# Kernel optimization log

Measured on AMD Instinct MI355X. Metric: run time of the kernel, lower is better.

The kernel has to match this reference:

```python
import jax, jax.numpy as jnp
import numpy as np

B, NMASK, DIM, HEADS = 8, 1024, 768, 12
HEAD_DIM = DIM // HEADS
SCALE = HEAD_DIM ** -0.5
NEG = -1e9  # finite stand-in for -inf to keep fully-masked rows NaN-free


def setup_inputs() -> dict:
    key = jax.random.key(0)
    ks = jax.random.split(key, 7)
    x = jax.random.normal(ks[0], (B, NMASK + 1, DIM), dtype=jnp.float32)
    # valid-prefix padding mask (realistic variable-length batch), lengths >= 1
    lengths = jax.random.randint(ks[1], (B,), 1, NMASK + 1)
    mask = jnp.arange(NMASK)[None, :] < lengths[:, None]  # (B, NMASK) bool
    w_qkv = jax.random.normal(ks[2], (DIM, 3 * DIM), dtype=jnp.float32) * (DIM ** -0.5)
    b_qkv = jax.random.normal(ks[3], (3 * DIM,), dtype=jnp.float32) * 0.02
    w_proj = jax.random.normal(ks[4], (DIM, DIM), dtype=jnp.float32) * (DIM ** -0.5)
    b_proj = jax.random.normal(ks[5], (DIM,), dtype=jnp.float32) * 0.02
    return {"x": x, "mask": mask, "w_qkv": w_qkv, "b_qkv": b_qkv,
            "w_proj": w_proj, "b_proj": b_proj}


def reference(x, mask, w_qkv, b_qkv, w_proj, b_proj):
    b, n, _ = x.shape
    qkv = x @ w_qkv + b_qkv                        # (b, n, 3*dim)
    qkv = qkv.reshape(b, n, 3, HEADS, HEAD_DIM)    # 'b n (qkv h d)'
    qkv = jnp.transpose(qkv, (2, 0, 3, 1, 4))      # (3, b, h, n, d)
    q, k, v = qkv[0], qkv[1], qkv[2]
    logits = jnp.einsum('bhid,bhjd->bhij', q, k) * SCALE
    m = jnp.pad(mask, ((0, 0), (1, 0)), constant_values=True)   # prepend CLS=True
    am = m[:, None, :] & m[:, :, None]             # (b, n, n)
    logits = jnp.where(am[:, None, :, :], logits, NEG)
    attn = jax.nn.softmax(logits, axis=-1)
    out = jnp.einsum('bhij,bhjd->bhid', attn, v)   # (b, h, n, d)
    out = jnp.transpose(out, (0, 2, 1, 3)).reshape(b, n, DIM)
    return out @ w_proj + b_proj                   # dropout is identity (eval/p=0)
```

## Files before the change

kernel.cpp:

```cpp
#include <hip/hip_runtime.h>
#include <stdint.h>

#define BATCH   8
#define NMASK_  1024
#define SEQ     1025
#define NPAD    1056
#define DIM     768
#define HEADS   12
#define HD      64
#define BHN     (BATCH*HEADS)
#define MROWS   (BATCH*SEQ)
#define K3      (3*DIM)

typedef unsigned short u16;
typedef __attribute__((ext_vector_type(8))) short s8v;
typedef __attribute__((ext_vector_type(4))) float f4v;
typedef __attribute__((ext_vector_type(4))) unsigned short u16x4;

__device__ __forceinline__ u16 rne_bf16(float f) {
  unsigned u = __float_as_uint(f);
  u += 0x7fffu + ((u >> 16) & 1u);
  return (u16)(u >> 16);
}
__device__ __forceinline__ float bf2f(u16 u) {
  return __uint_as_float(((unsigned)u) << 16);
}

__device__ __forceinline__ void gld16(const u16* g, u16* l) {
  __builtin_amdgcn_global_load_lds(
      (const __attribute__((address_space(1))) void*)g,
      (__attribute__((address_space(3))) void*)l, 16, 0, 0);
}

__global__ __launch_bounds__(256) void k_len(const int* __restrict__ mask,
                                             int* __restrict__ lens) {
  int b = blockIdx.x, t = threadIdx.x;
  int s = 0;
  for (int j = t; j < NMASK_; j += 256) s += (mask[b * NMASK_ + j] != 0) ? 1 : 0;
  __shared__ int red[256];
  red[t] = s; __syncthreads();
  for (int st = 128; st > 0; st >>= 1) { if (t < st) red[t] += red[t + st]; __syncthreads(); }
  if (t == 0) lens[b] = red[0] + 1;
}

__global__ __launch_bounds__(256) void k_cvt_x(const float* __restrict__ x,
                                               u16* __restrict__ xb, int n4) {
  int i = blockIdx.x * 256 + threadIdx.x;
  if (i >= n4) return;
  float4 v = ((const float4*)x)[i];
  u16x4 o;
  o[0] = rne_bf16(v.x); o[1] = rne_bf16(v.y); o[2] = rne_bf16(v.z); o[3] = rne_bf16(v.w);
  *(u16x4*)&xb[i * 4] = o;
}

__global__ __launch_bounds__(256) void k_wT(const float* __restrict__ w,
                                            u16* __restrict__ wT, int R, int C) {
  __shared__ float tile[32][33];
  int c0 = blockIdx.x * 32, r0 = blockIdx.y * 32;
  int tx = threadIdx.x & 31, ty = threadIdx.x >> 5;
  #pragma unroll
  for (int i = 0; i < 32; i += 8) tile[ty + i][tx] = w[(size_t)(r0 + ty + i) * C + c0 + tx];
  __syncthreads();
  #pragma unroll
  for (int i = 0; i < 32; i += 8)
    wT[(size_t)(c0 + ty + i) * R + r0 + tx] = rne_bf16(tile[tx][ty + i]);
}

__global__ __launch_bounds__(256) void k_zpad(u16* __restrict__ VT) {
  int idx = blockIdx.x * 256 + threadIdx.x;
  const int PADW = NPAD - SEQ;
  if (idx >= BHN * HD * PADW) return;
  int c = idx % PADW, rd = idx / PADW;
  VT[(size_t)rd * NPAD + SEQ + c] = 0;
}

__device__ __forceinline__ void gemm_ml128(const u16* __restrict__ A,
                                           const u16* __restrict__ Bt,
                                           int M, int m0, int n0,
                                           f4v acc[4][4], u16* smem) {
  u16* lA = smem;
  u16* lB = smem + 4096;
  const int t = threadIdx.x;
  const int w = t >> 6, l = t & 63, lg = l >> 4, lr = l & 15;
  const int wr = w >> 1, wc = w & 1;

  int rA0 = m0 + (t >> 2);       if (rA0 >= M) rA0 = M - 1;
  int rA1 = m0 + (t >> 2) + 64;  if (rA1 >= M) rA1 = M - 1;
  const u16* sA0 = A  + (size_t)rA0 * DIM + (t & 3) * 8;
  const u16* sA1 = A  + (size_t)rA1 * DIM + (t & 3) * 8;
  const u16* sB0 = Bt + (size_t)(n0 + (t >> 2)) * DIM + (t & 3) * 8;
  const u16* sB1 = Bt + (size_t)(n0 + (t >> 2) + 64) * DIM + (t & 3) * 8;
  u16* dA0 = &lA[w * 512];
  u16* dA1 = &lA[2048 + w * 512];
  u16* dB0 = &lB[w * 512];
  u16* dB1 = &lB[2048 + w * 512];

  #pragma unroll
  for (int fm = 0; fm < 4; fm++)
    #pragma unroll
    for (int fn = 0; fn < 4; fn++) { f4v z = {0.f, 0.f, 0.f, 0.f}; acc[fm][fn] = z; }

  for (int k0 = 0; k0 < DIM; k0 += 32) {
    __syncthreads();
    gld16(sA0, dA0); gld16(sA1, dA1);
    gld16(sB0, dB0); gld16(sB1, dB1);
    sA0 += 32; sA1 += 32; sB0 += 32; sB1 += 32;
    __syncthreads();
    s8v a[4], bb[4];
    #pragma unroll
    for (int fm = 0; fm < 4; fm++) a[fm] = *(const s8v*)&lA[(wr * 64 + fm * 16 + lr) * 32 + lg * 8];
    #pragma unroll
    for (int fn = 0; fn < 4; fn++) bb[fn] = *(const s8v*)&lB[(wc * 64 + fn * 16 + lr) * 32 + lg * 8];
    #pragma unroll
    for (int fm = 0; fm < 4; fm++)
      #pragma unroll
      for (int fn = 0; fn < 4; fn++)
        acc[fm][fn] = __builtin_amdgcn_mfma_f32_16x16x32_bf16(a[fm], bb[fn], acc[fm][fn], 0, 0, 0);
  }
}

__global__ __launch_bounds__(256) void k_gemm_qkv(const u16* __restrict__ xb,
                                                  const u16* __restrict__ wqkvT,
                                                  const float* __restrict__ bqkv,
                                                  const int* __restrict__ lens,
                                                  u16* __restrict__ Q,
                                                  u16* __restrict__ Kb,
                                                  u16* __restrict__ VT) {
  __shared__ alignas(16) u16 smem[16384];
  int m0 = blockIdx.x * 128, n0 = blockIdx.y * 128;
  const int which = n0 / DIM;
  if (which < 2) {
    int b0 = m0 / SEQ, off = m0 - b0 * SEQ;
    bool spans = (m0 + 127) >= (b0 + 1) * SEQ;
    if (!spans && off >= lens[b0]) return;
  }
  f4v acc[4][4];
  gemm_ml128(xb, wqkvT, MROWS, m0, n0, acc, smem);
  const int t = threadIdx.x;
  const int w = t >> 6, l = t & 63, lg = l >> 4, lr = l & 15;
  const int wr = w >> 1, wc = w & 1;
  const int hbase = (n0 - which * DIM) >> 6;
  const float qs = (which == 0) ? 0.125f : 1.0f;

  __syncthreads();
  #pragma unroll
  for (int fn = 0; fn < 4; fn++) {
    int col = wc * 64 + fn * 16 + lr;
    float bias = bqkv[n0 + col];
    #pragma unroll
    for (int fm = 0; fm < 4; fm++)
      #pragma unroll
      for (int r = 0; r < 4; r++) {
        int row = wr * 64 + fm * 16 + lg * 4 + r;
        smem[row * 128 + col] = rne_bf16((acc[fm][fn][r] + bias) * qs);
      }
  }
  __syncthreads();

  if (which < 2) {
    u16* dst = (which == 0) ? Q : Kb;
    #pragma unroll
    for (int p = 0; p < 8; p++) {
      int c = p * 256 + t;
      int row = c >> 4, col = (c & 15) * 8;
      int gm = m0 + row;
      if (gm >= MROWS) continue;
      int b = gm / SEQ, n = gm - b * SEQ;
      int head = hbase + (col >> 6), d = col & 63;
      *(s8v*)&dst[((size_t)(b * HEADS + head) * NPAD + n) * HD + d] =
          *(const s8v*)&smem[row * 128 + col];
    }
  } else {
    #pragma unroll
    for (int p = 0; p < 8; p++) {
      int c = p * 256 + t;
      int d = c & 127, nb = c >> 7;
      int gm0 = m0 + nb * 8;
      if (gm0 >= MROWS) continue;
      int head = hbase + (d >> 6), dl = d & 63;
      int b0 = gm0 / SEQ;
      if (gm0 + 7 < MROWS && (gm0 + 7) < (b0 + 1) * SEQ) {
        s8v v;
        #pragma unroll
        for (int e = 0; e < 8; e++) v[e] = (short)smem[(nb * 8 + e) * 128 + d];
        int n = gm0 - b0 * SEQ;
        *(s8v*)&VT[((size_t)(b0 * HEADS + head) * HD + dl) * NPAD + n] = v;
      } else {
        for (int e = 0; e < 8; e++) {
          int gm = gm0 + e;
          if (gm >= MROWS) break;
          int b = gm / SEQ, n = gm - b * SEQ;
          VT[((size_t)(b * HEADS + head) * HD + dl) * NPAD + n] = smem[(nb * 8 + e) * 128 + d];
        }
      }
    }
  }
}

__global__ __launch_bounds__(256) void k_vmean(const u16* __restrict__ VT,
                                               float* __restrict__ vmean) {
  int bh = blockIdx.x, t = threadIdx.x;
  int d = t >> 2, part = t & 3;
  const u16* row = VT + (size_t)(bh * HD + d) * NPAD;
  float s = 0.f;
  for (int jc = part * 264; jc < part * 264 + 264; jc += 8) {
    if (jc + 8 <= SEQ) {
      s8v v = *(const s8v*)&row[jc];
      #pragma unroll
      for (int e = 0; e < 8; e++) s += bf2f((u16)v[e]);
    } else {
      for (int e = 0; e < 8; e++) if (jc + e < SEQ) s += bf2f(row[jc + e]);
    }
  }
  __shared__ float red[256];
  red[t] = s; __syncthreads();
  if (part == 0)
    vmean[bh * HD + d] = (red[t] + red[t + 1] + red[t + 2] + red[t + 3]) * (1.0f / (float)SEQ);
}

__global__ __launch_bounds__(256) void k_vproj(const float* __restrict__ vmean,
                                               const u16* __restrict__ wprojT,
                                               const float* __restrict__ bproj,
                                               float* __restrict__ vproj) {
  int gid = blockIdx.x * 4 + (threadIdx.x >> 6);
  if (gid >= BATCH * DIM) return;
  int b = gid / DIM, n = gid - b * DIM;
  int l = threadIdx.x & 63;
  const u16* wr = wprojT + (size_t)n * DIM;
  const float* vm = vmean + b * DIM;
  float s = 0.f;
  #pragma unroll
  for (int i = 0; i < DIM / 64; ++i)
    s += vm[l + i * 64] * bf2f(wr[l + i * 64]);
  #pragma unroll
  for (int off = 32; off >= 1; off >>= 1) s += __shfl_xor(s, off);
  if (l == 0) vproj[gid] = s + bproj[n];
}

__global__ __launch_bounds__(256) void k_attn(const u16* __restrict__ Q,
                                              const u16* __restrict__ Kb,
                                              const u16* __restrict__ VT,
                                              const int* __restrict__ lens,
                                              u16* __restrict__ aout) {
  int bh = blockIdx.y; int b = bh / HEADS, h = bh - b * HEADS;
  int Lp1 = lens[b];
  int q0 = blockIdx.x * 64;
  if (q0 >= Lp1) return;
  __shared__ alignas(16) u16 Kt[64 * 64];
  __shared__ alignas(16) u16 Vt[64 * 64];
  __shared__ alignas(16) u16 Pt[4][16 * 72];
  const int t = threadIdx.x, w = t >> 6, l = t & 63, lg = l >> 4, lr = l & 15;
  const u16* Qbh = Q  + (size_t)bh * NPAD * HD;
  const u16* Kbh = Kb + (size_t)bh * NPAD * HD;
  const u16* Vbh = VT + (size_t)bh * HD * NPAD;

  int qi = q0 + w * 16 + lr;
  s8v qf[2];
  qf[0] = *(const s8v*)&Qbh[(size_t)qi * HD +      lg * 8];
  qf[1] = *(const s8v*)&Qbh[(size_t)qi * HD + 32 + lg * 8];

  f4v o[4];
  #pragma unroll
  for (int fd = 0; fd < 4; fd++) { f4v z = {0.f, 0.f, 0.f, 0.f}; o[fd] = z; }
  float mrow[4], ssum[4];
  #pragma unroll
  for (int r = 0; r < 4; r++) { mrow[r] = -1e30f; ssum[r] = 0.f; }

  const int js = t >> 2, cs = t & 3;
  const u16* kSrc = Kbh + (size_t)js * HD   + cs * 8;
  const u16* vSrc = Vbh + (size_t)js * NPAD + cs * 8;
  const int kDst0 = js * 64 + ((cs       ^ (js & 7)) * 8);
  const int kDst1 = js * 64 + (((cs + 4) ^ (js & 7)) * 8);
  s8v kr0, kr1, vr0, vr1;
  kr0 = *(const s8v*)(kSrc);        kr1 = *(const s8v*)(kSrc + 32);
  vr0 = *(const s8v*)(vSrc);        vr1 = *(const s8v*)(vSrc + 32);

  for (int j0 = 0; j0 < Lp1; j0 += 64) {
    __syncthreads();
    *(s8v*)&Kt[kDst0] = kr0;  *(s8v*)&Kt[kDst1] = kr1;
    *(s8v*)&Vt[kDst0] = vr0;  *(s8v*)&Vt[kDst1] = vr1;
    if (j0 + 64 < Lp1) {
      kr0 = *(const s8v*)(kSrc + (size_t)(j0 + 64) * HD);
      kr1 = *(const s8v*)(kSrc + (size_t)(j0 + 64) * HD + 32);
      vr0 = *(const s8v*)(vSrc + (j0 + 64));
      vr1 = *(const s8v*)(vSrc + (j0 + 64) + 32);
    }
    __syncthreads();

    f4v sf[4];
    #pragma unroll
    for (int jf = 0; jf < 4; jf++) { f4v z = {0.f,0.f,0.f,0.f}; sf[jf] = z; }
    __builtin_amdgcn_s_setprio(1);
    #pragma unroll
    for (int jf = 0; jf < 4; jf++) {
      int j = jf * 16 + lr;
      #pragma unroll
      for (int kf = 0; kf < 2; kf++) {
        s8v kfr = *(const s8v*)&Kt[j * 64 + (((kf * 4 + lg) ^ (j & 7)) * 8)];
        sf[jf] = __builtin_amdgcn_mfma_f32_16x16x32_bf16(qf[kf], kfr, sf[jf], 0, 0, 0);
      }
    }
    __builtin_amdgcn_s_setprio(0);

    bool ok[4];
    #pragma unroll
    for (int jf = 0; jf < 4; jf++) ok[jf] = (j0 + jf * 16 + lr) < Lp1;

    float sv[4][4], pmax[4];
    #pragma unroll
    for (int r = 0; r < 4; r++) {
      float s0 = ok[0] ? sf[0][r] : -1e30f;
      float s1 = ok[1] ? sf[1][r] : -1e30f;
      float s2 = ok[2] ? sf[2][r] : -1e30f;
      float s3 = ok[3] ? sf[3][r] : -1e30f;
      sv[r][0] = s0; sv[r][1] = s1; sv[r][2] = s2; sv[r][3] = s3;
      float tm = fmaxf(fmaxf(s0, s1), fmaxf(s2, s3));
      tm = fmaxf(tm, __shfl_xor(tm, 1)); tm = fmaxf(tm, __shfl_xor(tm, 2));
      tm = fmaxf(tm, __shfl_xor(tm, 4)); tm = fmaxf(tm, __shfl_xor(tm, 8));
      pmax[r] = tm;
    }
    bool ng = (pmax[0] <= mrow[0] + 8.f) && (pmax[1] <= mrow[1] + 8.f) &&
              (pmax[2] <= mrow[2] + 8.f) && (pmax[3] <= mrow[3] + 8.f);
    if (!__all(ng)) {
      #pragma unroll
      for (int r = 0; r < 4; r++) {
        float nm = fmaxf(mrow[r], pmax[r]);
        float fs = __expf(mrow[r] - nm);
        mrow[r] = nm;
        ssum[r] *= fs;
        o[0][r] *= fs; o[1][r] *= fs; o[2][r] *= fs; o[3][r] *= fs;
      }
    }
    u16* P = &Pt[w][0];
    #pragma unroll
    for (int r = 0; r < 4; r++) {
      float e0 = __expf(sv[r][0] - mrow[r]);
      float e1 = __expf(sv[r][1] - mrow[r]);
      float e2 = __expf(sv[r][2] - mrow[r]);
      float e3 = __expf(sv[r][3] - mrow[r]);
      int prow = (lg * 4 + r) * 72;
      P[prow +      lr] = rne_bf16(e0);
      P[prow + 16 + lr] = rne_bf16(e1);
      P[prow + 32 + lr] = rne_bf16(e2);
      P[prow + 48 + lr] = rne_bf16(e3);
      float rs = (e0 + e1) + (e2 + e3);
      rs += __shfl_xor(rs, 1); rs += __shfl_xor(rs, 2);
      rs += __shfl_xor(rs, 4); rs += __shfl_xor(rs, 8);
      ssum[r] += rs;
    }
    asm volatile("s_waitcnt lgkmcnt(0)" ::: "memory");
    s8v pa[2];
    pa[0] = *(const s8v*)&P[lr * 72 +      lg * 8];
    pa[1] = *(const s8v*)&P[lr * 72 + 32 + lg * 8];
    __builtin_amdgcn_s_setprio(1);
    #pragma unroll
    for (int fd = 0; fd < 4; fd++) {
      int dv = fd * 16 + lr;
      #pragma unroll
      for (int kf = 0; kf < 2; kf++) {
        s8v vb = *(const s8v*)&Vt[dv * 64 + (((kf * 4 + lg) ^ (dv & 7)) * 8)];
        o[fd] = __builtin_amdgcn_mfma_f32_16x16x32_bf16(pa[kf], vb, o[fd], 0, 0, 0);
      }
    }
    __builtin_amdgcn_s_setprio(0);
  }

  float inv[4];
  #pragma unroll
  for (int r = 0; r < 4; r++) inv[r] = 1.0f / ssum[r];
  #pragma unroll
  for (int fd = 0; fd < 4; fd++)
    #pragma unroll
    for (int r = 0; r < 4; r++) {
      int i = q0 + w * 16 + lg * 4 + r;
      if (i < Lp1)
        aout[(size_t)(b * SEQ + i) * DIM + h * HD + fd * 16 + lr] = rne_bf16(o[fd][r] * inv[r]);
    }
}

__global__ __launch_bounds__(256) void k_bcast(const int* __restrict__ lens,
                                               const float* __restrict__ vproj,
                                               float* __restrict__ out) {
  int idx = blockIdx.x * 256 + threadIdx.x;
  if (idx >= MROWS * DIM / 4) return;
  int e4 = idx * 4;
  int b = e4 / (SEQ * DIM);
  int rem = e4 - b * (SEQ * DIM);
  int i = rem / DIM;
  if (i >= lens[b]) {
    int c = rem - i * DIM;
    const float* vp = &vproj[b * DIM + c];
    float4 v = { vp[0], vp[1], vp[2], vp[3] };
    ((float4*)out)[idx] = v;
  }
}

__global__ __launch_bounds__(256) void k_gemm_proj(const u16* __restrict__ aout,
                                                   const u16* __restrict__ wprojT,
                                                   const float* __restrict__ bproj,
                                                   const int* __restrict__ lens,
                                                   float* __restrict__ out) {
  __shared__ alignas(16) u16 smem[16384];
  int m0 = blockIdx.x * 128, n0 = blockIdx.y * 128;
  {
    int b0 = m0 / SEQ, off = m0 - b0 * SEQ;
    bool spans = (m0 + 127) >= (b0 + 1) * SEQ;
    if (!spans && off >= lens[b0]) return;
  }
  f4v acc[4][4];
  gemm_ml128(aout, wprojT, MROWS, m0, n0, acc, smem);
  const int t = threadIdx.x;
  const int w = t >> 6, l = t & 63, lg = l >> 4, lr = l & 15;
  const int wr = w >> 1, wc = w & 1;
  #pragma unroll
  for (int fn = 0; fn < 4; fn++) {
    int gc = n0 + wc * 64 + fn * 16 + lr;
    float bias = bproj[gc];
    #pragma unroll
    for (int fm = 0; fm < 4; fm++)
      #pragma unroll
      for (int r = 0; r < 4; r++) {
        int gm = m0 + wr * 64 + fm * 16 + lg * 4 + r;
        if (gm < MROWS) out[(size_t)gm * DIM + gc] = acc[fm][fn][r] + bias;
      }
  }
}

extern "C" void kernel_launch(void* const* d_in, const int* in_sizes, int n_in,
                              void* d_out, int out_size, void* d_ws, size_t ws_size,
                              hipStream_t stream) {
  const float* x      = (const float*)d_in[0];
  const int*   mask   = (const int*)  d_in[1];
  const float* w_qkv  = (const float*)d_in[2];
  const float* b_qkv  = (const float*)d_in[3];
  const float* w_proj = (const float*)d_in[4];
  const float* b_proj = (const float*)d_in[5];
  float* out = (float*)d_out;

  u16* xb     = (u16*)d_ws;
  u16* wqkvT  = xb    + (size_t)MROWS * DIM;
  u16* wprojT = wqkvT + (size_t)K3 * DIM;
  u16* Q      = wprojT + (size_t)DIM * DIM;
  u16* Kb     = Q     + (size_t)BHN * NPAD * HD;
  u16* VT     = Kb    + (size_t)BHN * NPAD * HD;
  float* vmean = (float*)(VT + (size_t)BHN * NPAD * HD);
  int* lens    = (int*)(vmean + BHN * HD);
  float* vproj = (float*)(lens + 256);
  u16* aout   = xb;

  k_len  <<<dim3(BATCH), dim3(256), 0, stream>>>(mask, lens);
  k_cvt_x<<<dim3((MROWS * DIM / 4 + 255) / 256), dim3(256), 0, stream>>>(x, xb, MROWS * DIM / 4);
  k_wT   <<<dim3(K3 / 32, DIM / 32), dim3(256), 0, stream>>>(w_qkv, wqkvT, DIM, K3);
  k_wT   <<<dim3(DIM / 32, DIM / 32), dim3(256), 0, stream>>>(w_proj, wprojT, DIM, DIM);
  k_zpad <<<dim3((BHN * HD * (NPAD - SEQ) + 255) / 256), dim3(256), 0, stream>>>(VT);
  k_gemm_qkv<<<dim3((MROWS + 127) / 128, K3 / 128), dim3(256), 0, stream>>>(xb, wqkvT, b_qkv, lens, Q, Kb, VT);
  k_vmean<<<dim3(BHN), dim3(256), 0, stream>>>(VT, vmean);
  k_vproj<<<dim3((BATCH * DIM + 3) / 4), dim3(256), 0, stream>>>(vmean, wprojT, b_proj, vproj);
  k_attn <<<dim3((SEQ + 63) / 64, BHN), dim3(256), 0, stream>>>(Q, Kb, VT, lens, aout);
  k_gemm_proj<<<dim3((MROWS + 127) / 128, DIM / 128), dim3(256), 0, stream>>>(aout, wprojT, b_proj, lens, out);
  k_bcast<<<dim3((MROWS * DIM / 4 + 255) / 256), dim3(256), 0, stream>>>(lens, vproj, out);
}
```

Baseline: 185.2 us.

## Process 128 query rows per attention block, reusing each K/V tile twice

Each wave in the attention kernel now handles two 16-row query sub-tiles instead of one, so a block covers 128 queries. Every K/V tile loaded into shared memory, and every V fragment read from it, serves twice as many MFMAs, which halves global K/V traffic and syncs per query. The grid is also reordered so bh is the fast dimension, spreading the variable-length batches across CUs. The cost is more registers per thread and fewer blocks, about 9 per head, which may lower occupancy and worsen load balance.

```diff
diff --git a/kernel.cpp b/kernel.cpp
--- a/kernel.cpp
+++ b/kernel.cpp
@@ -242,29 +242,36 @@
                                               const u16* __restrict__ VT,
                                               const int* __restrict__ lens,
                                               u16* __restrict__ aout) {
-  int bh = blockIdx.y; int b = bh / HEADS, h = bh - b * HEADS;
+  int bh = blockIdx.x; int b = bh / HEADS, h = bh - b * HEADS;
   int Lp1 = lens[b];
-  int q0 = blockIdx.x * 64;
+  int q0 = blockIdx.y * 128;
   if (q0 >= Lp1) return;
   __shared__ alignas(16) u16 Kt[64 * 64];
   __shared__ alignas(16) u16 Vt[64 * 64];
-  __shared__ alignas(16) u16 Pt[4][16 * 72];
+  __shared__ alignas(16) u16 Pt[4][32 * 72];
   const int t = threadIdx.x, w = t >> 6, l = t & 63, lg = l >> 4, lr = l & 15;
   const u16* Qbh = Q  + (size_t)bh * NPAD * HD;
   const u16* Kbh = Kb + (size_t)bh * NPAD * HD;
   const u16* Vbh = VT + (size_t)bh * HD * NPAD;
 
-  int qi = q0 + w * 16 + lr;
-  s8v qf[2];
-  qf[0] = *(const s8v*)&Qbh[(size_t)qi * HD +      lg * 8];
-  qf[1] = *(const s8v*)&Qbh[(size_t)qi * HD + 32 + lg * 8];
-
-  f4v o[4];
-  #pragma unroll
-  for (int fd = 0; fd < 4; fd++) { f4v z = {0.f, 0.f, 0.f, 0.f}; o[fd] = z; }
-  float mrow[4], ssum[4];
-  #pragma unroll
-  for (int r = 0; r < 4; r++) { mrow[r] = -1e30f; ssum[r] = 0.f; }
+  s8v qf[2][2];
+  #pragma unroll
+  for (int qa = 0; qa < 2; qa++) {
+    int qi = q0 + w * 32 + qa * 16 + lr;
+    qf[qa][0] = *(const s8v*)&Qbh[(size_t)qi * HD +      lg * 8];
+    qf[qa][1] = *(const s8v*)&Qbh[(size_t)qi * HD + 32 + lg * 8];
+  }
+
+  f4v o[2][4];
+  float mrow[2][4], ssum[2][4];
+  #pragma unroll
+  for (int qa = 0; qa < 2; qa++)
+    #pragma unroll
+    for (int fd = 0; fd < 4; fd++) { f4v z = {0.f, 0.f, 0.f, 0.f}; o[qa][fd] = z; }
+  #pragma unroll
+  for (int qa = 0; qa < 2; qa++)
+    #pragma unroll
+    for (int r = 0; r < 4; r++) { mrow[qa][r] = -1e30f; ssum[qa][r] = 0.f; }
 
   const int js = t >> 2, cs = t & 3;
   const u16* kSrc = Kbh + (size_t)js * HD   + cs * 8;
@@ -287,95 +294,107 @@
     }
     __syncthreads();
 
-    f4v sf[4];
-    #pragma unroll
-    for (int jf = 0; jf < 4; jf++) { f4v z = {0.f,0.f,0.f,0.f}; sf[jf] = z; }
-    __builtin_amdgcn_s_setprio(1);
-    #pragma unroll
-    for (int jf = 0; jf < 4; jf++) {
-      int j = jf * 16 + lr;
-      #pragma unroll
-      for (int kf = 0; kf < 2; kf++) {
-        s8v kfr = *(const s8v*)&Kt[j * 64 + (((kf * 4 + lg) ^ (j & 7)) * 8)];
-        sf[jf] = __builtin_amdgcn_mfma_f32_16x16x32_bf16(qf[kf], kfr, sf[jf], 0, 0, 0);
-      }
-    }
-    __builtin_amdgcn_s_setprio(0);
-
     bool ok[4];
     #pragma unroll
     for (int jf = 0; jf < 4; jf++) ok[jf] = (j0 + jf * 16 + lr) < Lp1;
-
-    float sv[4][4], pmax[4];
-    #pragma unroll
-    for (int r = 0; r < 4; r++) {
-      float s0 = ok[0] ? sf[0][r] : -1e30f;
-      float s1 = ok[1] ? sf[1][r] : -1e30f;
-      float s2 = ok[2] ? sf[2][r] : -1e30f;
-      float s3 = ok[3] ? sf[3][r] : -1e30f;
-      sv[r][0] = s0; sv[r][1] = s1; sv[r][2] = s2; sv[r][3] = s3;
-      float tm = fmaxf(fmaxf(s0, s1), fmaxf(s2, s3));
-      tm = fmaxf(tm, __shfl_xor(tm, 1)); tm = fmaxf(tm, __shfl_xor(tm, 2));
-      tm = fmaxf(tm, __shfl_xor(tm, 4)); tm = fmaxf(tm, __shfl_xor(tm, 8));
-      pmax[r] = tm;
-    }
-    bool ng = (pmax[0] <= mrow[0] + 8.f) && (pmax[1] <= mrow[1] + 8.f) &&
-              (pmax[2] <= mrow[2] + 8.f) && (pmax[3] <= mrow[3] + 8.f);
-    if (!__all(ng)) {
+    u16* P = &Pt[w][0];
+
+    #pragma unroll
+    for (int qa = 0; qa < 2; qa++) {
+      f4v sf[4];
+      #pragma unroll
+      for (int jf = 0; jf < 4; jf++) { f4v z = {0.f,0.f,0.f,0.f}; sf[jf] = z; }
+      __builtin_amdgcn_s_setprio(1);
+      #pragma unroll
+      for (int jf = 0; jf < 4; jf++) {
+        int j = jf * 16 + lr;
+        #pragma unroll
+        for (int kf = 0; kf < 2; kf++) {
+          s8v kfr = *(const s8v*)&Kt[j * 64 + (((kf * 4 + lg) ^ (j & 7)) * 8)];
+          sf[jf] = __builtin_amdgcn_mfma_f32_16x16x32_bf16(qf[qa][kf], kfr, sf[jf], 0, 0, 0);
+        }
+      }
+      __builtin_amdgcn_s_setprio(0);
+
+      float sv[4][4], pmax[4];
       #pragma unroll
       for (int r = 0; r < 4; r++) {
-        float nm = fmaxf(mrow[r], pmax[r]);
-        float fs = __expf(mrow[r] - nm);
-        mrow[r] = nm;
-        ssum[r] *= fs;
-        o[0][r] *= fs; o[1][r] *= fs; o[2][r] *= fs; o[3][r] *= fs;
-      }
-    }
-    u16* P = &Pt[w][0];
-    #pragma unroll
-    for (int r = 0; r < 4; r++) {
-      float e0 = __expf(sv[r][0] - mrow[r]);
-      float e1 = __expf(sv[r][1] - mrow[r]);
-      float e2 = __expf(sv[r][2] - mrow[r]);
-      float e3 = __expf(sv[r][3] - mrow[r]);
-      int prow = (lg * 4 + r) * 72;
-      P[prow +      lr] = rne_bf16(e0);
-      P[prow + 16 + lr] = rne_bf16(e1);
-      P[prow + 32 + lr] = rne_bf16(e2);
-      P[prow + 48 + lr] = rne_bf16(e3);
-      float rs = (e0 + e1) + (e2 + e3);
-      rs += __shfl_xor(rs, 1); rs += __shfl_xor(rs, 2);
-      rs += __shfl_xor(rs, 4); rs += __shfl_xor(rs, 8);
-      ssum[r] += rs;
-    }
+        float s0 = ok[0] ? sf[0][r] : -1e30f;
+        float s1 = ok[1] ? sf[1][r] : -1e30f;
+        float s2 = ok[2] ? sf[2][r] : -1e30f;
+        float s3 = ok[3] ? sf[3][r] : -1e30f;
+        sv[r][0] = s0; sv[r][1] = s1; sv[r][2] = s2; sv[r][3] = s3;
+        float tm = fmaxf(fmaxf(s0, s1), fmaxf(s2, s3));
+        tm = fmaxf(tm, __shfl_xor(tm, 1)); tm = fmaxf(tm, __shfl_xor(tm, 2));
+        tm = fmaxf(tm, __shfl_xor(tm, 4)); tm = fmaxf(tm, __shfl_xor(tm, 8));
+        pmax[r] = tm;
+      }
+      bool ng = (pmax[0] <= mrow[qa][0] + 8.f) && (pmax[1] <= mrow[qa][1] + 8.f) &&
+                (pmax[2] <= mrow[qa][2] + 8.f) && (pmax[3] <= mrow[qa][3] + 8.f);
+      if (!__all(ng)) {
+        #pragma unroll
+        for (int r = 0; r < 4; r++) {
+          float nm = fmaxf(mrow[qa][r], pmax[r]);
+          float fs = __expf(mrow[qa][r] - nm);
+          mrow[qa][r] = nm;
+          ssum[qa][r] *= fs;
+          o[qa][0][r] *= fs; o[qa][1][r] *= fs; o[qa][2][r] *= fs; o[qa][3][r] *= fs;
+        }
+      }
+      #pragma unroll
+      for (int r = 0; r < 4; r++) {
+        float e0 = __expf(sv[r][0] - mrow[qa][r]);
+        float e1 = __expf(sv[r][1] - mrow[qa][r]);
+        float e2 = __expf(sv[r][2] - mrow[qa][r]);
+        float e3 = __expf(sv[r][3] - mrow[qa][r]);
+        int prow = (qa * 16 + lg * 4 + r) * 72;
+        P[prow +      lr] = rne_bf16(e0);
+        P[prow + 16 + lr] = rne_bf16(e1);
+        P[prow + 32 + lr] = rne_bf16(e2);
+        P[prow + 48 + lr] = rne_bf16(e3);
+        float rs = (e0 + e1) + (e2 + e3);
+        rs += __shfl_xor(rs, 1); rs += __shfl_xor(rs, 2);
+        rs += __shfl_xor(rs, 4); rs += __shfl_xor(rs, 8);
+        ssum[qa][r] += rs;
+      }
+    }
+
     asm volatile("s_waitcnt lgkmcnt(0)" ::: "memory");
-    s8v pa[2];
-    pa[0] = *(const s8v*)&P[lr * 72 +      lg * 8];
-    pa[1] = *(const s8v*)&P[lr * 72 + 32 + lg * 8];
+    s8v pa[2][2];
+    #pragma unroll
+    for (int qa = 0; qa < 2; qa++) {
+      pa[qa][0] = *(const s8v*)&P[(qa * 16 + lr) * 72 +      lg * 8];
+      pa[qa][1] = *(const s8v*)&P[(qa * 16 + lr) * 72 + 32 + lg * 8];
+    }
     __builtin_amdgcn_s_setprio(1);
     #pragma unroll
     for (int fd = 0; fd < 4; fd++) {
       int dv = fd * 16 + lr;
-      #pragma unroll
-      for (int kf = 0; kf < 2; kf++) {
-        s8v vb = *(const s8v*)&Vt[dv * 64 + (((kf * 4 + lg) ^ (dv & 7)) * 8)];
-        o[fd] = __builtin_amdgcn_mfma_f32_16x16x32_bf16(pa[kf], vb, o[fd], 0, 0, 0);
+      s8v vb0 = *(const s8v*)&Vt[dv * 64 + (((0 * 4 + lg) ^ (dv & 7)) * 8)];
+      s8v vb1 = *(const s8v*)&Vt[dv * 64 + (((1 * 4 + lg) ^ (dv & 7)) * 8)];
+      #pragma unroll
+      for (int qa = 0; qa < 2; qa++) {
+        o[qa][fd] = __builtin_amdgcn_mfma_f32_16x16x32_bf16(pa[qa][0], vb0, o[qa][fd], 0, 0, 0);
+        o[qa][fd] = __builtin_amdgcn_mfma_f32_16x16x32_bf16(pa[qa][1], vb1, o[qa][fd], 0, 0, 0);
       }
     }
     __builtin_amdgcn_s_setprio(0);
   }
 
-  float inv[4];
-  #pragma unroll
-  for (int r = 0; r < 4; r++) inv[r] = 1.0f / ssum[r];
-  #pragma unroll
-  for (int fd = 0; fd < 4; fd++)
-    #pragma unroll
-    for (int r = 0; r < 4; r++) {
-      int i = q0 + w * 16 + lg * 4 + r;
-      if (i < Lp1)
-        aout[(size_t)(b * SEQ + i) * DIM + h * HD + fd * 16 + lr] = rne_bf16(o[fd][r] * inv[r]);
-    }
+  #pragma unroll
+  for (int qa = 0; qa < 2; qa++) {
+    float inv[4];
+    #pragma unroll
+    for (int r = 0; r < 4; r++) inv[r] = 1.0f / ssum[qa][r];
+    #pragma unroll
+    for (int fd = 0; fd < 4; fd++)
+      #pragma unroll
+      for (int r = 0; r < 4; r++) {
+        int i = q0 + w * 32 + qa * 16 + lg * 4 + r;
+        if (i < Lp1)
+          aout[(size_t)(b * SEQ + i) * DIM + h * HD + fd * 16 + lr] = rne_bf16(o[qa][fd][r] * inv[r]);
+      }
+  }
 }
 
 __global__ __launch_bounds__(256) void k_bcast(const int* __restrict__ lens,
@@ -456,7 +475,7 @@
   k_gemm_qkv<<<dim3((MROWS + 127) / 128, K3 / 128), dim3(256), 0, stream>>>(xb, wqkvT, b_qkv, lens, Q, Kb, VT);
   k_vmean<<<dim3(BHN), dim3(256), 0, stream>>>(VT, vmean);
   k_vproj<<<dim3((BATCH * DIM + 3) / 4), dim3(256), 0, stream>>>(vmean, wprojT, b_proj, vproj);
-  k_attn <<<dim3((SEQ + 63) / 64, BHN), dim3(256), 0, stream>>>(Q, Kb, VT, lens, aout);
+  k_attn <<<dim3(BHN, (SEQ + 127) / 128), dim3(256), 0, stream>>>(Q, Kb, VT, lens, aout);
   k_gemm_proj<<<dim3((MROWS + 127) / 128, DIM / 128), dim3(256), 0, stream>>>(aout, wprojT, b_proj, lens, out);
   k_bcast<<<dim3((MROWS * DIM / 4 + 255) / 256), dim3(256), 0, stream>>>(lens, vproj, out);
 }
```

New measurement: 208.7 us. 1.13x slower.
